# Kernel tuning notes

Hardware: AMD Instinct MI355X
Metric: run time of the kernel (lower is better)

## Reference

```python
import jax, jax.numpy as jnp
import numpy as np

D_MODEL = 1024
N_HEADS = 16
D_K = D_MODEL // N_HEADS
D_FF = 4096
B, S = 2, 2048
EPS = 1e-5
SCALE = 0.02


def setup_inputs() -> dict:
    key = jax.random.key(0)
    ks = jax.random.split(key, 8)
    return {
        "x": jax.random.normal(ks[0], (B, S, D_MODEL), dtype=jnp.float32),
        "ln1_w": jnp.ones((D_MODEL,), jnp.float32),
        "ln1_b": jnp.zeros((D_MODEL,), jnp.float32),
        "Wq": jax.random.normal(ks[1], (D_MODEL, D_MODEL), jnp.float32) * SCALE,
        "bq": jnp.zeros((D_MODEL,), jnp.float32),
        "Wk": jax.random.normal(ks[2], (D_MODEL, D_MODEL), jnp.float32) * SCALE,
        "bk": jnp.zeros((D_MODEL,), jnp.float32),
        "Wv": jax.random.normal(ks[3], (D_MODEL, D_MODEL), jnp.float32) * SCALE,
        "bv": jnp.zeros((D_MODEL,), jnp.float32),
        "Wo": jax.random.normal(ks[4], (D_MODEL, D_MODEL), jnp.float32) * SCALE,
        "bo": jnp.zeros((D_MODEL,), jnp.float32),
        "ln2_w": jnp.ones((D_MODEL,), jnp.float32),
        "ln2_b": jnp.zeros((D_MODEL,), jnp.float32),
        "W1": jax.random.normal(ks[5], (D_MODEL, D_FF), jnp.float32) * SCALE,
        "b1": jnp.zeros((D_FF,), jnp.float32),
        "W2": jax.random.normal(ks[6], (D_FF, D_MODEL), jnp.float32) * SCALE,
        "b2": jnp.zeros((D_MODEL,), jnp.float32),
    }


def _layernorm(x, w, b):
    mu = jnp.mean(x, axis=-1, keepdims=True)
    var = jnp.mean(jnp.square(x - mu), axis=-1, keepdims=True)
    return (x - mu) * jax.lax.rsqrt(var + EPS) * w + b


def reference(x, ln1_w, ln1_b, Wq, bq, Wk, bk, Wv, bv, Wo, bo,
              ln2_w, ln2_b, W1, b1, W2, b2):
    # Pre-norm multi-head self-attention (dropout = identity, eval mode)
    h = _layernorm(x, ln1_w, ln1_b)                      # [B,S,D]
    q = (h @ Wq + bq).reshape(B, S, N_HEADS, D_K)        # [B,S,H,Dk]
    k = (h @ Wk + bk).reshape(B, S, N_HEADS, D_K)
    v = (h @ Wv + bv).reshape(B, S, N_HEADS, D_K)
    scores = jnp.einsum('bqhd,bkhd->bhqk', q, k) / jnp.sqrt(jnp.float32(D_K))
    attn = jax.nn.softmax(scores, axis=-1)               # [B,H,S,S]
    ctx = jnp.einsum('bhqk,bkhd->bqhd', attn, v).reshape(B, S, D_MODEL)
    x = x + (ctx @ Wo + bo)
    # Pre-norm FFN
    h2 = _layernorm(x, ln2_w, ln2_b)
    ff = jax.nn.relu(h2 @ W1 + b1) @ W2 + b2
    return x + ff
```

## Files before the change

### kernel.cpp

```cpp
#include <hip/hip_runtime.h>
#include <hip/hip_bf16.h>
#include <cstdint>
#include <cstddef>

typedef unsigned short ushort_t;
typedef __bf16 bf16x8 __attribute__((ext_vector_type(8)));
typedef float f32x4 __attribute__((ext_vector_type(4)));

#define D_MODEL 1024
#define D_FF 4096
#define BB 2
#define SS 2048
#define NH 16
#define MROWS (BB * SS)
#define KVBLK 64

__device__ __forceinline__ ushort_t f2bf(float f) {
  union { float f; unsigned u; } x; x.f = f;
  unsigned r = x.u + 0x7fffu + ((x.u >> 16) & 1u);
  return (ushort_t)(r >> 16);
}

__device__ __forceinline__ void gload_lds16(const void* g, void* l) {
  __builtin_amdgcn_global_load_lds((const __attribute__((address_space(1))) void*)g,
                                   (__attribute__((address_space(3))) void*)l, 16, 0, 0);
}

__device__ __forceinline__ float dpp_sum16(float x) {
  int v;
  v = __builtin_amdgcn_update_dpp(0, __float_as_int(x), 0xB1, 0xF, 0xF, true);
  x += __int_as_float(v);
  v = __builtin_amdgcn_update_dpp(0, __float_as_int(x), 0x4E, 0xF, 0xF, true);
  x += __int_as_float(v);
  v = __builtin_amdgcn_update_dpp(0, __float_as_int(x), 0x141, 0xF, 0xF, true);
  x += __int_as_float(v);
  v = __builtin_amdgcn_update_dpp(0, __float_as_int(x), 0x140, 0xF, 0xF, true);
  x += __int_as_float(v);
  return x;
}

__global__ __launch_bounds__(256) void ln_bf16_kernel(
    const float* __restrict__ x, const float* __restrict__ w,
    const float* __restrict__ b, ushort_t* __restrict__ out) {
  int row = blockIdx.x;
  int tid = threadIdx.x;
  int lane = tid & 63, wid = tid >> 6;
  const float4 v = ((const float4*)(x + (size_t)row * D_MODEL))[tid];
  float s = v.x + v.y + v.z + v.w;
  __shared__ float red[8];
  #pragma unroll
  for (int o = 32; o > 0; o >>= 1) s += __shfl_down(s, o);
  if (lane == 0) red[wid] = s;
  __syncthreads();
  float mu = (red[0] + red[1] + red[2] + red[3]) * (1.0f / D_MODEL);
  float d0 = v.x - mu, d1 = v.y - mu, d2 = v.z - mu, d3 = v.w - mu;
  float sq = d0 * d0 + d1 * d1 + d2 * d2 + d3 * d3;
  #pragma unroll
  for (int o = 32; o > 0; o >>= 1) sq += __shfl_down(sq, o);
  if (lane == 0) red[4 + wid] = sq;
  __syncthreads();
  float var = (red[4] + red[5] + red[6] + red[7]) * (1.0f / D_MODEL);
  float rstd = rsqrtf(var + 1e-5f);
  const float4 wv = ((const float4*)w)[tid];
  const float4 bv = ((const float4*)b)[tid];
  ushort4 o4;
  o4.x = f2bf(d0 * rstd * wv.x + bv.x);
  o4.y = f2bf(d1 * rstd * wv.y + bv.y);
  o4.z = f2bf(d2 * rstd * wv.z + bv.z);
  o4.w = f2bf(d3 * rstd * wv.w + bv.w);
  ((ushort4*)(out + (size_t)row * D_MODEL))[tid] = o4;
}

__global__ __launch_bounds__(256) void transpose_cast_kernel(
    const float* __restrict__ W, ushort_t* __restrict__ Wt, int K, int N) {
  __shared__ float tile[32][33];
  int bx = blockIdx.x * 32;
  int by = blockIdx.y * 32;
  int tx = threadIdx.x, ty = threadIdx.y;
  #pragma unroll
  for (int i = 0; i < 32; i += 8)
    tile[ty + i][tx] = W[(size_t)(by + ty + i) * N + bx + tx];
  __syncthreads();
  #pragma unroll
  for (int i = 0; i < 32; i += 8)
    Wt[(size_t)(bx + ty + i) * K + by + tx] = f2bf(tile[tx][ty + i]);
}

__global__ __launch_bounds__(256) void vtrans_kernel(
    const ushort_t* __restrict__ qkv, ushort_t* __restrict__ Vt) {
  __shared__ __align__(16) ushort_t T[64 * 64];
  const int tid = threadIdx.x;
  const int bh = blockIdx.y, b = bh >> 4, h = bh & 15;
  const int kv0 = blockIdx.x * 64;
  const ushort_t* Vp = qkv + (size_t)b * SS * 3072 + 2048 + h * 64;
  #pragma unroll
  for (int i = 0; i < 2; i++) {
    int idx = tid * 2 + i;
    int key = idx >> 3, c = idx & 7;
    bf16x8 v = *(const bf16x8*)(Vp + (size_t)(kv0 + key) * 3072 + c * 8);
    *(bf16x8*)(T + key * 64 + ((c ^ (key & 7)) * 8)) = v;
  }
  __syncthreads();
  int d = tid >> 2, kb = tid & 3;
  ushort_t o[16];
  #pragma unroll
  for (int j = 0; j < 16; j++) {
    int key = kb * 16 + j;
    o[j] = T[key * 64 + (((d >> 3) ^ (key & 7)) * 8) + (d & 7)];
  }
  ushort_t* dst = Vt + (size_t)(bh * 64 + d) * SS + kv0 + kb * 16;
  *(bf16x8*)dst = *(bf16x8*)&o[0];
  *(bf16x8*)(dst + 8) = *(bf16x8*)&o[8];
}

template <int EPI>
__global__ __launch_bounds__(256, 2) void gemm128_kernel(
    const ushort_t* __restrict__ A, const ushort_t* __restrict__ Bt,
    const float* __restrict__ bias, const float* __restrict__ resid,
    void* __restrict__ Cout, int M, int N, int K, int NTn, int Ksplit, int MTN) {
  __shared__ __align__(16) ushort_t lds[4][2][4096];
  const int tid = threadIdx.x, lane = tid & 63, wid = tid >> 6;
  const int wm = wid >> 1, wn = wid & 1;
  const int rl = lane & 15, cg = lane >> 4;
  int nwg = gridDim.x;
  int q = nwg >> 3, rr = nwg & 7;
  int xcd = blockIdx.x & 7, idx = blockIdx.x >> 3;
  int wgid = (xcd < rr ? xcd * (q + 1) : rr * (q + 1) + (xcd - rr) * q) + idx;
  const int s = wgid / MTN;
  int rem = wgid - s * MTN;
  const int row0 = (rem / NTn) * 128, col0 = (rem - (rem / NTn) * NTn) * 128;
  const int k0 = s * Ksplit;
  const int NT = Ksplit / 32;

  int soff[2], ldso[2];
  #pragma unroll
  for (int i = 0; i < 2; i++) {
    int ci = wid * 128 + i * 64 + lane;
    int P = ci * 16;
    int L = P ^ (((P >> 7) & 7) << 4);
    int row = L >> 6, kc = (L >> 4) & 3;
    soff[i] = row * K + kc * 8;
    ldso[i] = (wid * 128 + i * 64) * 8;
  }

  f32x4 acc[4][4] = {};

  auto stage = [&](int t) {
    int b = t & 3;
    int kk = k0 + t * 32;
    #pragma unroll
    for (int i = 0; i < 2; i++) {
      gload_lds16(A + (size_t)row0 * K + kk + soff[i], &lds[b][0][ldso[i]]);
      gload_lds16(Bt + (size_t)col0 * K + kk + soff[i], &lds[b][1][ldso[i]]);
    }
  };

  auto compute = [&](int t) {
    int b = t & 3;
    bf16x8 af[4], bfv[4];
    #pragma unroll
    for (int mi = 0; mi < 4; mi++) {
      int r = wm * 64 + mi * 16 + rl;
      int L = r * 64 + cg * 16;
      int P = L ^ (((L >> 7) & 7) << 4);
      af[mi] = *(const bf16x8*)&lds[b][0][P >> 1];
    }
    #pragma unroll
    for (int ni = 0; ni < 4; ni++) {
      int r = wn * 64 + ni * 16 + rl;
      int L = r * 64 + cg * 16;
      int P = L ^ (((L >> 7) & 7) << 4);
      bfv[ni] = *(const bf16x8*)&lds[b][1][P >> 1];
    }
    __builtin_amdgcn_s_setprio(1);
    #pragma unroll
    for (int mi = 0; mi < 4; mi++)
      #pragma unroll
      for (int ni = 0; ni < 4; ni++)
        acc[mi][ni] = __builtin_amdgcn_mfma_f32_16x16x32_bf16(af[mi], bfv[ni], acc[mi][ni], 0, 0, 0);
    __builtin_amdgcn_s_setprio(0);
  };

  stage(0); stage(1); stage(2);
  for (int t = 0; t < NT; ++t) {
    if (t < NT - 2)       asm volatile("s_waitcnt vmcnt(8)" ::: "memory");
    else if (t == NT - 2) asm volatile("s_waitcnt vmcnt(4)" ::: "memory");
    else                  asm volatile("s_waitcnt vmcnt(0)" ::: "memory");
    __builtin_amdgcn_s_barrier();
    __builtin_amdgcn_sched_barrier(0);
    if (t + 3 < NT) stage(t + 3);
    compute(t);
  }

  if (EPI == 2) {
    float* out = (float*)Cout;
    #pragma unroll
    for (int ni = 0; ni < 4; ni++) {
      int col = col0 + wn * 64 + ni * 16 + rl;
      float bv = bias[col];
      #pragma unroll
      for (int mi = 0; mi < 4; mi++) {
        int rowb = row0 + wm * 64 + mi * 16 + cg * 4;
        #pragma unroll
        for (int j = 0; j < 4; j++)
          out[(size_t)(rowb + j) * N + col] =
              acc[mi][ni][j] + bv + resid[(size_t)(rowb + j) * N + col];
      }
    }
  } else if (EPI == 3) {
    float* out = (float*)Cout + (size_t)s * M * N;
    #pragma unroll
    for (int ni = 0; ni < 4; ni++) {
      int col = col0 + wn * 64 + ni * 16 + rl;
      #pragma unroll
      for (int mi = 0; mi < 4; mi++) {
        int rowb = row0 + wm * 64 + mi * 16 + cg * 4;
        #pragma unroll
        for (int j = 0; j < 4; j++)
          out[(size_t)(rowb + j) * N + col] = acc[mi][ni][j];
      }
    }
  } else {
    ushort_t* out = (ushort_t*)Cout;
    #pragma unroll
    for (int ni = 0; ni < 4; ni++) {
      int col = col0 + wn * 64 + ni * 16 + rl;
      float bv = bias[col];
      float sc = (EPI == 0 && col < 1024) ? 0.18033688011f : 1.0f;
      #pragma unroll
      for (int mi = 0; mi < 4; mi++) {
        int rowb = row0 + wm * 64 + mi * 16 + cg * 4;
        #pragma unroll
        for (int j = 0; j < 4; j++) {
          float v = acc[mi][ni][j] + bv;
          if (EPI == 1) v = fmaxf(v, 0.0f);
          if (EPI == 0) v *= sc;
          out[(size_t)(rowb + j) * N + col] = f2bf(v);
        }
      }
    }
  }
}

__global__ __launch_bounds__(256) void reduce_kernel(
    const float* __restrict__ p, const float* __restrict__ bias,
    const float* __restrict__ resid, float* __restrict__ out,
    int S, size_t total4, size_t stride4) {
  const float4* p4 = (const float4*)p;
  const float4* r4 = (const float4*)resid;
  const float4* b4 = (const float4*)bias;
  float4* o4 = (float4*)out;
  for (size_t i = (size_t)blockIdx.x * 256 + threadIdx.x; i < total4;
       i += (size_t)gridDim.x * 256) {
    float4 a = r4[i];
    float4 bb = b4[i & 255];
    a.x += bb.x; a.y += bb.y; a.z += bb.z; a.w += bb.w;
    for (int s = 0; s < S; ++s) {
      float4 v = p4[(size_t)s * stride4 + i];
      a.x += v.x; a.y += v.y; a.z += v.z; a.w += v.w;
    }
    o4[i] = a;
  }
}

__global__ __launch_bounds__(256) void attn_kernel(
    const ushort_t* __restrict__ qkv, const ushort_t* __restrict__ Vt,
    ushort_t* __restrict__ ctx) {
  __shared__ __align__(16) ushort_t Kl[2][64 * 64];
  __shared__ __align__(16) ushort_t Vl[2][64 * 64];
  __shared__ __align__(16) ushort_t Pl[4][16 * 64];
  const int tid = threadIdx.x, lane = tid & 63, wid = tid >> 6;
  int bid = blockIdx.y * 32 + blockIdx.x;
  int w = (bid & 7) * 128 + (bid >> 3);
  const int bh = w >> 5, qt = w & 31;
  const int b = bh >> 4, h = bh & 15;
  const int q0 = qt * 64 + wid * 16;
  const ushort_t* Qp = qkv + (size_t)b * SS * 3072 + h * 64;
  const ushort_t* Kp = Qp + 1024;
  const ushort_t* Vg = Vt + (size_t)bh * 64 * SS;

  bf16x8 qf[2];
  {
    int qr = q0 + (lane & 15);
    #pragma unroll
    for (int s2 = 0; s2 < 2; s2++)
      qf[s2] = *(const bf16x8*)(Qp + (size_t)qr * 3072 + s2 * 32 + (lane >> 4) * 8);
  }
  float l[4];
  f32x4 acc[4] = {};
  #pragma unroll
  for (int r = 0; r < 4; r++) l[r] = 0.f;

  const int NT = SS / KVBLK;

  int ksrc[2], vsrc[2];
  #pragma unroll
  for (int i = 0; i < 2; i++) {
    int idx = wid * 128 + i * 64 + lane;
    int R = idx >> 3, c = idx & 7;
    int key = (R & 15) * 4 + (R >> 4);
    ksrc[i] = key * 3072 + ((c ^ (R & 7)) * 8);
    vsrc[i] = R * SS + ((c ^ (R & 7)) * 8);
  }
  const int ldsb = wid * 1024;

  auto stageKV = [&](int buf, int t) {
    size_t kvK = (size_t)t * KVBLK * 3072;
    int kvV = t * KVBLK;
    gload_lds16(Kp + kvK + ksrc[0], &Kl[buf][ldsb]);
    gload_lds16(Kp + kvK + ksrc[1], &Kl[buf][ldsb + 512]);
    gload_lds16(Vg + kvV + vsrc[0], &Vl[buf][ldsb]);
    gload_lds16(Vg + kvV + vsrc[1], &Vl[buf][ldsb + 512]);
  };

  auto body = [&](int t, int cb) {
    __syncthreads();
    if (t + 1 < NT) stageKV(cb ^ 1, t + 1);

    f32x4 s4[4] = {};
    #pragma unroll
    for (int g = 0; g < 4; g++) {
      const ushort_t* kr = &Kl[cb][(g * 16 + (lane & 15)) * 64];
      bf16x8 kf0 = *(const bf16x8*)(kr + (((lane >> 4)) ^ ((lane & 15) & 7)) * 8);
      bf16x8 kf1 = *(const bf16x8*)(kr + ((4 + (lane >> 4)) ^ ((lane & 15) & 7)) * 8);
      s4[g] = __builtin_amdgcn_mfma_f32_16x16x32_bf16(qf[0], kf0, s4[g], 0, 0, 0);
      s4[g] = __builtin_amdgcn_mfma_f32_16x16x32_bf16(qf[1], kf1, s4[g], 0, 0, 0);
    }
    const int qrow = (lane >> 4) * 4;
    const int cp = (lane & 15) >> 1, hf = (lane & 15) & 1;
    #pragma unroll
    for (int r = 0; r < 4; r++) {
      float p0 = __builtin_amdgcn_exp2f(s4[0][r]);
      float p1 = __builtin_amdgcn_exp2f(s4[1][r]);
      float p2 = __builtin_amdgcn_exp2f(s4[2][r]);
      float p3 = __builtin_amdgcn_exp2f(s4[3][r]);
      l[r] += (p0 + p1) + (p2 + p3);
      unsigned w0, w1;
      asm("v_cvt_pk_bf16_f32 %0, %1, %2" : "=v"(w0) : "v"(p0), "v"(p1));
      asm("v_cvt_pk_bf16_f32 %0, %1, %2" : "=v"(w1) : "v"(p2), "v"(p3));
      uint2 pw; pw.x = w0; pw.y = w1;
      int qq = qrow + r;
      *(uint2*)(&Pl[wid][qq * 64 + ((cp ^ (qq & 7)) * 8) + hf * 4]) = pw;
    }
    asm volatile("s_waitcnt lgkmcnt(0)" ::: "memory");
    __builtin_amdgcn_sched_barrier(0);
    bf16x8 pf[2];
    {
      int qq = lane & 15;
      #pragma unroll
      for (int ks = 0; ks < 2; ks++) {
        int c = ks * 4 + (lane >> 4);
        pf[ks] = *(const bf16x8*)(&Pl[wid][qq * 64 + ((c ^ (qq & 7)) * 8)]);
      }
    }
    #pragma unroll
    for (int f = 0; f < 4; f++) {
      int d = f * 16 + (lane & 15);
      #pragma unroll
      for (int ks = 0; ks < 2; ks++) {
        int chunk = (ks * 4 + (lane >> 4)) ^ (d & 7);
        bf16x8 vf = *(const bf16x8*)(&Vl[cb][d * 64 + chunk * 8]);
        acc[f] = __builtin_amdgcn_mfma_f32_16x16x32_bf16(pf[ks], vf, acc[f], 0, 0, 0);
      }
    }
  };

  stageKV(0, 0);
  for (int t = 0; t < NT; t += 2) {
    body(t, 0);
    body(t + 1, 1);
  }

  #pragma unroll
  for (int r = 0; r < 4; r++) l[r] = dpp_sum16(l[r]);
  float rl4[4];
  #pragma unroll
  for (int r = 0; r < 4; r++) rl4[r] = 1.0f / l[r];
  #pragma unroll
  for (int f = 0; f < 4; f++)
    #pragma unroll
    for (int r = 0; r < 4; r++) {
      int row = b * SS + q0 + (lane >> 4) * 4 + r;
      int col = h * 64 + f * 16 + (lane & 15);
      ctx[(size_t)row * D_MODEL + col] = f2bf(acc[f][r] * rl4[r]);
    }
}

extern "C" void kernel_launch(void* const* d_in, const int* in_sizes, int n_in,
                              void* d_out, int out_size, void* d_ws, size_t ws_size,
                              hipStream_t stream) {
  const float* x    = (const float*)d_in[0];
  const float* ln1w = (const float*)d_in[1];
  const float* ln1b = (const float*)d_in[2];
  const float* Wq   = (const float*)d_in[3];
  const float* bq   = (const float*)d_in[4];
  const float* Wk   = (const float*)d_in[5];
  const float* bk   = (const float*)d_in[6];
  const float* Wv   = (const float*)d_in[7];
  const float* bv   = (const float*)d_in[8];
  const float* Wo   = (const float*)d_in[9];
  const float* bo   = (const float*)d_in[10];
  const float* ln2w = (const float*)d_in[11];
  const float* ln2b = (const float*)d_in[12];
  const float* W1   = (const float*)d_in[13];
  const float* b1   = (const float*)d_in[14];
  const float* W2   = (const float*)d_in[15];
  const float* b2   = (const float*)d_in[16];

  char* ws = (char*)d_ws;
  size_t off = 0;
  auto alloc = [&](size_t bytes) {
    void* p = ws + off;
    off += (bytes + 255) & ~(size_t)255;
    return p;
  };
  ushort_t* Wt_qkv = (ushort_t*)alloc((size_t)3072 * 1024 * 2);
  ushort_t* Wt_o   = (ushort_t*)alloc((size_t)1024 * 1024 * 2);
  ushort_t* Wt_1   = (ushort_t*)alloc((size_t)4096 * 1024 * 2);
  ushort_t* Wt_2   = (ushort_t*)alloc((size_t)1024 * 4096 * 2);
  float*    bqkv   = (float*)alloc((size_t)3072 * 4);
  ushort_t* qkvb   = (ushort_t*)alloc((size_t)MROWS * 3072 * 2);
  ushort_t* ctxb   = (ushort_t*)alloc((size_t)MROWS * 1024 * 2);
  ushort_t* hbuf   = (ushort_t*)alloc((size_t)MROWS * 1024 * 2);
  float*    x2     = (float*)alloc((size_t)MROWS * 1024 * 4);
  ushort_t* Vtb    = (ushort_t*)alloc((size_t)BB * NH * 64 * SS * 2);
  ushort_t* ff1    = qkvb;
  float*    outp   = (float*)d_out;

  const size_t partial1 = (size_t)MROWS * 1024 * 4;
  int S = (ws_size - off >= 2 * partial1 + 256) ? 2 : 1;
  float* pbuf = (S == 2) ? (float*)alloc(2 * partial1) : nullptr;

  dim3 tb(32, 8);
  transpose_cast_kernel<<<dim3(32, 32), tb, 0, stream>>>(Wq, Wt_qkv, 1024, 1024);
  transpose_cast_kernel<<<dim3(32, 32), tb, 0, stream>>>(Wk, Wt_qkv + 1024 * 1024, 1024, 1024);
  transpose_cast_kernel<<<dim3(32, 32), tb, 0, stream>>>(Wv, Wt_qkv + 2 * 1024 * 1024, 1024, 1024);
  transpose_cast_kernel<<<dim3(32, 32), tb, 0, stream>>>(Wo, Wt_o, 1024, 1024);
  transpose_cast_kernel<<<dim3(128, 32), tb, 0, stream>>>(W1, Wt_1, 1024, 4096);
  transpose_cast_kernel<<<dim3(32, 128), tb, 0, stream>>>(W2, Wt_2, 4096, 1024);
  hipMemcpyAsync(bqkv,        bq, 1024 * 4, hipMemcpyDeviceToDevice, stream);
  hipMemcpyAsync(bqkv + 1024, bk, 1024 * 4, hipMemcpyDeviceToDevice, stream);
  hipMemcpyAsync(bqkv + 2048, bv, 1024 * 4, hipMemcpyDeviceToDevice, stream);

  ln_bf16_kernel<<<MROWS, 256, 0, stream>>>(x, ln1w, ln1b, hbuf);
  gemm128_kernel<0><<<dim3(24 * 32), 256, 0, stream>>>(
      hbuf, Wt_qkv, bqkv, nullptr, qkvb, MROWS, 3072, 1024, 24, 1024, 24 * 32);
  vtrans_kernel<<<dim3(SS / 64, BB * NH), 256, 0, stream>>>(qkvb, Vtb);
  attn_kernel<<<dim3(SS / 64, BB * NH), 256, 0, stream>>>(qkvb, Vtb, ctxb);
  gemm128_kernel<2><<<dim3(8 * 32), 256, 0, stream>>>(
      ctxb, Wt_o, bo, x, x2, MROWS, 1024, 1024, 8, 1024, 8 * 32);
  ln_bf16_kernel<<<MROWS, 256, 0, stream>>>(x2, ln2w, ln2b, hbuf);
  gemm128_kernel<1><<<dim3(32 * 32), 256, 0, stream>>>(
      hbuf, Wt_1, b1, nullptr, ff1, MROWS, D_FF, 1024, 32, 1024, 32 * 32);
  if (S == 2) {
    gemm128_kernel<3><<<dim3(8 * 32 * 2), 256, 0, stream>>>(
        ff1, Wt_2, nullptr, nullptr, pbuf, MROWS, 1024, 4096, 8, 2048, 8 * 32);
    reduce_kernel<<<2048, 256, 0, stream>>>(pbuf, b2, x2, outp, 2,
        (size_t)MROWS * 1024 / 4, (size_t)MROWS * 1024 / 4);
  } else {
    gemm128_kernel<2><<<dim3(8 * 32), 256, 0, stream>>>(
        ff1, Wt_2, b2, x2, outp, MROWS, 1024, 4096, 8, 4096, 8 * 32);
  }
}
```

Baseline: 253.5 us.

## Rewrite attention with 32x32x16 MFMA, S^T layout, and permlane P repack

The attention kernel switches from 16x16x32 MFMAs to 32x32x16 MFMAs, computing transposed scores (K as A operand) so each wave handles 32 query rows and each block 128 queries. The P matrix is repacked into the B-operand layout in registers with v_permlane32_swap instead of a round trip through LDS, and the per-wave P shared buffer is removed. Row sums are reduced with one lane shuffle and shared through a small LDS table. This doubles K/V reuse per block and removes LDS traffic for P, at the cost of higher register pressure and half as many blocks.

```diff
diff --git a/kernel.cpp b/kernel.cpp
--- a/kernel.cpp
+++ b/kernel.cpp
@@ -6,6 +6,7 @@
 typedef unsigned short ushort_t;
 typedef __bf16 bf16x8 __attribute__((ext_vector_type(8)));
 typedef float f32x4 __attribute__((ext_vector_type(4)));
+typedef float f32x16 __attribute__((ext_vector_type(16)));
 
 #define D_MODEL 1024
 #define D_FF 4096
@@ -26,17 +27,10 @@
                                    (__attribute__((address_space(3))) void*)l, 16, 0, 0);
 }
 
-__device__ __forceinline__ float dpp_sum16(float x) {
-  int v;
-  v = __builtin_amdgcn_update_dpp(0, __float_as_int(x), 0xB1, 0xF, 0xF, true);
-  x += __int_as_float(v);
-  v = __builtin_amdgcn_update_dpp(0, __float_as_int(x), 0x4E, 0xF, 0xF, true);
-  x += __int_as_float(v);
-  v = __builtin_amdgcn_update_dpp(0, __float_as_int(x), 0x141, 0xF, 0xF, true);
-  x += __int_as_float(v);
-  v = __builtin_amdgcn_update_dpp(0, __float_as_int(x), 0x140, 0xF, 0xF, true);
-  x += __int_as_float(v);
-  return x;
+__device__ __forceinline__ bf16x8 pack4w(unsigned w0, unsigned w1, unsigned w2, unsigned w3) {
+  union { unsigned u[4]; bf16x8 v; } t;
+  t.u[0] = w0; t.u[1] = w1; t.u[2] = w2; t.u[3] = w3;
+  return t.v;
 }
 
 __global__ __launch_bounds__(256) void ln_bf16_kernel(
@@ -268,28 +262,27 @@
     ushort_t* __restrict__ ctx) {
   __shared__ __align__(16) ushort_t Kl[2][64 * 64];
   __shared__ __align__(16) ushort_t Vl[2][64 * 64];
-  __shared__ __align__(16) ushort_t Pl[4][16 * 64];
+  __shared__ float Lt[4][32];
   const int tid = threadIdx.x, lane = tid & 63, wid = tid >> 6;
-  int bid = blockIdx.y * 32 + blockIdx.x;
-  int w = (bid & 7) * 128 + (bid >> 3);
-  const int bh = w >> 5, qt = w & 31;
+  int bid = blockIdx.y * 16 + blockIdx.x;
+  int w = (bid & 7) * 64 + (bid >> 3);
+  const int bh = w >> 4, qt = w & 15;
   const int b = bh >> 4, h = bh & 15;
-  const int q0 = qt * 64 + wid * 16;
+  const int q0w = qt * 128 + wid * 32;
+  const int k31 = lane & 31, sg = lane >> 5, x7 = k31 & 7;
   const ushort_t* Qp = qkv + (size_t)b * SS * 3072 + h * 64;
   const ushort_t* Kp = Qp + 1024;
   const ushort_t* Vg = Vt + (size_t)bh * 64 * SS;
 
-  bf16x8 qf[2];
+  bf16x8 qf[4];
   {
-    int qr = q0 + (lane & 15);
-    #pragma unroll
-    for (int s2 = 0; s2 < 2; s2++)
-      qf[s2] = *(const bf16x8*)(Qp + (size_t)qr * 3072 + s2 * 32 + (lane >> 4) * 8);
-  }
-  float l[4];
-  f32x4 acc[4] = {};
-  #pragma unroll
-  for (int r = 0; r < 4; r++) l[r] = 0.f;
+    const ushort_t* qb = Qp + (size_t)(q0w + k31) * 3072 + sg * 8;
+    #pragma unroll
+    for (int dsl = 0; dsl < 4; dsl++)
+      qf[dsl] = *(const bf16x8*)(qb + dsl * 16);
+  }
+  float lsum = 0.f;
+  f32x16 o0 = {}, o1 = {};
 
   const int NT = SS / KVBLK;
 
@@ -298,8 +291,7 @@
   for (int i = 0; i < 2; i++) {
     int idx = wid * 128 + i * 64 + lane;
     int R = idx >> 3, c = idx & 7;
-    int key = (R & 15) * 4 + (R >> 4);
-    ksrc[i] = key * 3072 + ((c ^ (R & 7)) * 8);
+    ksrc[i] = R * 3072 + ((c ^ (R & 7)) * 8);
     vsrc[i] = R * SS + ((c ^ (R & 7)) * 8);
   }
   const int ldsb = wid * 1024;
@@ -313,55 +305,51 @@
     gload_lds16(Vg + kvV + vsrc[1], &Vl[buf][ldsb + 512]);
   };
 
+  auto softmax_half = [&](const f32x16& s, bf16x8& paE, bf16x8& paO) {
+    float pv[16];
+    #pragma unroll
+    for (int r = 0; r < 16; r++) pv[r] = __builtin_amdgcn_exp2f(s[r]);
+    #pragma unroll
+    for (int r = 0; r < 16; r++) lsum += pv[r];
+    unsigned W[4][2];
+    #pragma unroll
+    for (int qd = 0; qd < 4; qd++) {
+      asm("v_cvt_pk_bf16_f32 %0, %1, %2" : "=v"(W[qd][0]) : "v"(pv[4 * qd]), "v"(pv[4 * qd + 1]));
+      asm("v_cvt_pk_bf16_f32 %0, %1, %2" : "=v"(W[qd][1]) : "v"(pv[4 * qd + 2]), "v"(pv[4 * qd + 3]));
+    }
+    unsigned a0 = W[1][0], b0 = W[0][0], a1 = W[1][1], b1 = W[0][1];
+    asm("v_permlane32_swap_b32 %0, %1" : "+v"(a0), "+v"(b0));
+    asm("v_permlane32_swap_b32 %0, %1" : "+v"(a1), "+v"(b1));
+    paE = pack4w(b0, b1, a0, a1);
+    unsigned a2 = W[3][0], b2 = W[2][0], a3 = W[3][1], b3 = W[2][1];
+    asm("v_permlane32_swap_b32 %0, %1" : "+v"(a2), "+v"(b2));
+    asm("v_permlane32_swap_b32 %0, %1" : "+v"(a3), "+v"(b3));
+    paO = pack4w(b2, b3, a2, a3);
+  };
+
   auto body = [&](int t, int cb) {
     __syncthreads();
     if (t + 1 < NT) stageKV(cb ^ 1, t + 1);
 
-    f32x4 s4[4] = {};
-    #pragma unroll
-    for (int g = 0; g < 4; g++) {
-      const ushort_t* kr = &Kl[cb][(g * 16 + (lane & 15)) * 64];
-      bf16x8 kf0 = *(const bf16x8*)(kr + (((lane >> 4)) ^ ((lane & 15) & 7)) * 8);
-      bf16x8 kf1 = *(const bf16x8*)(kr + ((4 + (lane >> 4)) ^ ((lane & 15) & 7)) * 8);
-      s4[g] = __builtin_amdgcn_mfma_f32_16x16x32_bf16(qf[0], kf0, s4[g], 0, 0, 0);
-      s4[g] = __builtin_amdgcn_mfma_f32_16x16x32_bf16(qf[1], kf1, s4[g], 0, 0, 0);
-    }
-    const int qrow = (lane >> 4) * 4;
-    const int cp = (lane & 15) >> 1, hf = (lane & 15) & 1;
-    #pragma unroll
-    for (int r = 0; r < 4; r++) {
-      float p0 = __builtin_amdgcn_exp2f(s4[0][r]);
-      float p1 = __builtin_amdgcn_exp2f(s4[1][r]);
-      float p2 = __builtin_amdgcn_exp2f(s4[2][r]);
-      float p3 = __builtin_amdgcn_exp2f(s4[3][r]);
-      l[r] += (p0 + p1) + (p2 + p3);
-      unsigned w0, w1;
-      asm("v_cvt_pk_bf16_f32 %0, %1, %2" : "=v"(w0) : "v"(p0), "v"(p1));
-      asm("v_cvt_pk_bf16_f32 %0, %1, %2" : "=v"(w1) : "v"(p2), "v"(p3));
-      uint2 pw; pw.x = w0; pw.y = w1;
-      int qq = qrow + r;
-      *(uint2*)(&Pl[wid][qq * 64 + ((cp ^ (qq & 7)) * 8) + hf * 4]) = pw;
-    }
-    asm volatile("s_waitcnt lgkmcnt(0)" ::: "memory");
-    __builtin_amdgcn_sched_barrier(0);
-    bf16x8 pf[2];
-    {
-      int qq = lane & 15;
-      #pragma unroll
-      for (int ks = 0; ks < 2; ks++) {
-        int c = ks * 4 + (lane >> 4);
-        pf[ks] = *(const bf16x8*)(&Pl[wid][qq * 64 + ((c ^ (qq & 7)) * 8)]);
-      }
-    }
-    #pragma unroll
-    for (int f = 0; f < 4; f++) {
-      int d = f * 16 + (lane & 15);
-      #pragma unroll
-      for (int ks = 0; ks < 2; ks++) {
-        int chunk = (ks * 4 + (lane >> 4)) ^ (d & 7);
-        bf16x8 vf = *(const bf16x8*)(&Vl[cb][d * 64 + chunk * 8]);
-        acc[f] = __builtin_amdgcn_mfma_f32_16x16x32_bf16(pf[ks], vf, acc[f], 0, 0, 0);
-      }
+    f32x16 s0 = {}, s1 = {};
+    #pragma unroll
+    for (int dsl = 0; dsl < 4; dsl++) {
+      int ch = ((dsl * 2 + sg) ^ x7) * 8;
+      bf16x8 kf0 = *(const bf16x8*)(&Kl[cb][k31 * 64 + ch]);
+      bf16x8 kf1 = *(const bf16x8*)(&Kl[cb][(32 + k31) * 64 + ch]);
+      s0 = __builtin_amdgcn_mfma_f32_32x32x16_bf16(kf0, qf[dsl], s0, 0, 0, 0);
+      s1 = __builtin_amdgcn_mfma_f32_32x32x16_bf16(kf1, qf[dsl], s1, 0, 0, 0);
+    }
+    bf16x8 pa[4];
+    softmax_half(s0, pa[0], pa[1]);
+    softmax_half(s1, pa[2], pa[3]);
+    #pragma unroll
+    for (int ks = 0; ks < 4; ks++) {
+      int ch = ((2 * ks + sg) ^ x7) * 8;
+      bf16x8 vf0 = *(const bf16x8*)(&Vl[cb][k31 * 64 + ch]);
+      bf16x8 vf1 = *(const bf16x8*)(&Vl[cb][(32 + k31) * 64 + ch]);
+      o0 = __builtin_amdgcn_mfma_f32_32x32x16_bf16(pa[ks], vf0, o0, 0, 0, 0);
+      o1 = __builtin_amdgcn_mfma_f32_32x32x16_bf16(pa[ks], vf1, o1, 0, 0, 0);
     }
   };
 
@@ -371,19 +359,20 @@
     body(t + 1, 1);
   }
 
-  #pragma unroll
-  for (int r = 0; r < 4; r++) l[r] = dpp_sum16(l[r]);
-  float rl4[4];
-  #pragma unroll
-  for (int r = 0; r < 4; r++) rl4[r] = 1.0f / l[r];
-  #pragma unroll
-  for (int f = 0; f < 4; f++)
-    #pragma unroll
-    for (int r = 0; r < 4; r++) {
-      int row = b * SS + q0 + (lane >> 4) * 4 + r;
-      int col = h * 64 + f * 16 + (lane & 15);
-      ctx[(size_t)row * D_MODEL + col] = f2bf(acc[f][r] * rl4[r]);
-    }
+  float ltot = lsum + __shfl_xor(lsum, 32);
+  if (lane < 32) Lt[wid][lane] = ltot;
+  asm volatile("s_waitcnt lgkmcnt(0)" ::: "memory");
+  __builtin_amdgcn_sched_barrier(0);
+
+  const int colb = h * 64 + k31;
+  #pragma unroll
+  for (int r = 0; r < 16; r++) {
+    int qp = (r & 3) + 8 * (r >> 2) + 4 * sg;
+    float rlq = 1.0f / Lt[wid][qp];
+    size_t row = (size_t)(b * SS + q0w + qp);
+    ctx[row * D_MODEL + colb] = f2bf(o0[r] * rlq);
+    ctx[row * D_MODEL + colb + 32] = f2bf(o1[r] * rlq);
+  }
 }
 
 extern "C" void kernel_launch(void* const* d_in, const int* in_sizes, int n_in,
@@ -446,7 +435,7 @@
   gemm128_kernel<0><<<dim3(24 * 32), 256, 0, stream>>>(
       hbuf, Wt_qkv, bqkv, nullptr, qkvb, MROWS, 3072, 1024, 24, 1024, 24 * 32);
   vtrans_kernel<<<dim3(SS / 64, BB * NH), 256, 0, stream>>>(qkvb, Vtb);
-  attn_kernel<<<dim3(SS / 64, BB * NH), 256, 0, stream>>>(qkvb, Vtb, ctxb);
+  attn_kernel<<<dim3(SS / 128, BB * NH), 256, 0, stream>>>(qkvb, Vtb, ctxb);
   gemm128_kernel<2><<<dim3(8 * 32), 256, 0, stream>>>(
       ctxb, Wt_o, bo, x, x2, MROWS, 1024, 1024, 8, 1024, 8 * 32);
   ln_bf16_kernel<<<MROWS, 256, 0, stream>>>(x2, ln2w, ln2b, hbuf);
```

Result: faster. 246.1 us (-2.9%).
